# Performance work log

Measured on AMD Instinct MI355X. Metric: run time of the kernel, lower is better.

## Reference

```python
import jax, jax.numpy as jnp
import numpy as np

B, N, F, F1 = 1024, 75, 512, 256
NEG = -1.0e9
ALPHA = 0.2  # LeakyReLU slope


def setup_inputs() -> dict:
    key = jax.random.key(0)
    k1, k2, k3, k4 = jax.random.split(key, 4)
    X = jax.random.normal(k1, (B, N, F), dtype=jnp.float32)
    A = jax.random.randint(k2, (N, N), 0, 2, dtype=jnp.int32)  # binary adjacency
    W = jax.random.normal(k3, (F, F1), dtype=jnp.float32) * (1.0 / np.sqrt(F))
    a = jax.random.normal(k4, (2, F1, 1), dtype=jnp.float32) * (1.0 / np.sqrt(F1))
    return {"X": X, "A": A, "W": W, "a": a}


def reference(X, A, W, a):
    # Linear projection: [B, N, F1]
    h = jnp.einsum('bnf,fo->bno', X, W)
    # Additive attention logits
    att_self = jnp.einsum('bno,od->bnd', h, a[0])        # [B, N, 1]
    att_neigh = jnp.einsum('bno,od->bnd', h, a[1])       # [B, N, 1]
    e = att_self + jnp.swapaxes(att_neigh, 1, 2)         # [B, N, N]
    e = jax.nn.leaky_relu(e, ALPHA)
    # Adjacency mask: disallowed edges get large negative bias
    adj = A.astype(h.dtype)                               # [N, N]
    e = e + NEG * (1.0 - adj)[None, :, :]
    # Normalize over neighbors, aggregate
    alpha = jax.nn.softmax(e, axis=-1)                    # [B, N, N]
    out = jnp.einsum('bij,bjo->bio', alpha, h)            # [B, N, F1]
    return jnp.concatenate([out, h], axis=-1)             # [B, N, 2*F1]
```

## Files before the change

### kernel.cpp

```cpp
#include <hip/hip_runtime.h>
#include <hip/hip_bf16.h>
#include <math.h>

typedef __bf16 bf16_t;
typedef __bf16 bf16x4_t __attribute__((ext_vector_type(4)));
typedef __bf16 bf16x8 __attribute__((ext_vector_type(8)));
typedef float f32x4 __attribute__((ext_vector_type(4)));
typedef unsigned long long u64;

#define NB 1024
#define NN 75
#define KF 512
#define F1 256
#define HSTR 100
#define ASTR 100

__global__ __launch_bounds__(256) void wt_kernel(const float* __restrict__ W,
                                                 bf16_t* __restrict__ Wt) {
    __shared__ float tile[64][65];
    const int kb = blockIdx.x * 64;
    const int nb = blockIdx.y * 64;
    const int tc = threadIdx.x & 63;
    const int tr = threadIdx.x >> 6;
#pragma unroll
    for (int r = tr; r < 64; r += 4)
        tile[r][tc] = W[(size_t)(kb + r) * F1 + nb + tc];
    __syncthreads();
#pragma unroll
    for (int r = tr; r < 64; r += 4)
        Wt[(size_t)(nb + r) * KF + kb + tc] = (bf16_t)tile[tc][r];
}

__global__ __launch_bounds__(256) void gemm_kernel(const float* __restrict__ X,
                                                   const bf16_t* __restrict__ Wt,
                                                   float* __restrict__ out) {
    __shared__ __align__(16) bf16_t Asm[64 * 32];
    __shared__ __align__(16) bf16_t Bsm[256 * 32];
    const int t = threadIdx.x;
    const int w = t >> 6;
    const int l = t & 63;
    const int m0 = blockIdx.x * 64;

    f32x4 acc[16];
#pragma unroll
    for (int i = 0; i < 16; ++i) acc[i] = (f32x4){0.f, 0.f, 0.f, 0.f};

    const int ar = t >> 2;
    const int ak = (t & 3) * 8;
    const float* xptr = X + (size_t)(m0 + ar) * KF + ak;

    const int koff = (l >> 4) * 8;
    const bf16_t* afrag_p = &Asm[(w * 16 + (l & 15)) * 32 + koff];
    const bf16_t* bfrag_p = &Bsm[(l & 15) * 32 + koff];

    for (int ks = 0; ks < 16; ++ks) {
        const int k0 = ks * 32;
        const float4 x0 = *(const float4*)(xptr + k0);
        const float4 x1 = *(const float4*)(xptr + k0 + 4);
        bf16x8 av;
        av[0] = (bf16_t)x0.x; av[1] = (bf16_t)x0.y;
        av[2] = (bf16_t)x0.z; av[3] = (bf16_t)x0.w;
        av[4] = (bf16_t)x1.x; av[5] = (bf16_t)x1.y;
        av[6] = (bf16_t)x1.z; av[7] = (bf16_t)x1.w;
        *(bf16x8*)&Asm[ar * 32 + ak] = av;
#pragma unroll
        for (int p = 0; p < 4; ++p) {
            const int row = p * 64 + ar;
            *(uint4*)&Bsm[row * 32 + ak] =
                *(const uint4*)(Wt + (size_t)row * KF + k0 + ak);
        }
        __syncthreads();
        const bf16x8 af = *(const bf16x8*)afrag_p;
#pragma unroll
        for (int nt = 0; nt < 16; ++nt) {
            const bf16x8 bfv = *(const bf16x8*)(bfrag_p + nt * 16 * 32);
            acc[nt] = __builtin_amdgcn_mfma_f32_16x16x32_bf16(af, bfv, acc[nt], 0, 0, 0);
        }
        __syncthreads();
    }

    const int mrow = m0 + w * 16 + (l >> 4) * 4;
    const int ncol = l & 15;
#pragma unroll
    for (int nt = 0; nt < 16; ++nt) {
#pragma unroll
        for (int j = 0; j < 4; ++j) {
            out[(size_t)(mrow + j) * 512 + 256 + nt * 16 + ncol] = acc[nt][j];
        }
    }
}

__global__ __launch_bounds__(256) void pv_kernel(const int* __restrict__ Adj,
                                                 const float* __restrict__ avec,
                                                 float* __restrict__ out) {
    __shared__ __align__(16) bf16_t hT[256 * HSTR];
    __shared__ __align__(16) bf16_t alp[80 * ASTR];
    __shared__ float a0s[F1], a1s[F1];
    __shared__ float attp0[4][80], attp1[4][80];
    __shared__ float att0s[80], att1s[80], rsums[80];
    __shared__ u64 adjb[160];

    const int b = blockIdx.x;
    const int t = threadIdx.x;
    const int w = t >> 6;
    const int l = t & 63;
    const int lc = l & 15;
    const int lr = l >> 4;
    float* outb = out + (size_t)b * NN * 512;

    a0s[t] = avec[t];
    a1s[t] = avec[F1 + t];
    for (int i = w; i < NN; i += 4) {
        const int v0 = Adj[i * NN + l];
        const int v1 = (l < NN - 64) ? Adj[i * NN + 64 + l] : 0;
        const u64 b0 = __ballot(v0 != 0);
        const u64 b1 = __ballot(v1 != 0);
        if (l == 0) { adjb[i * 2] = b0; adjb[i * 2 + 1] = b1; }
    }
    {
        int* z = (int*)&hT[t * HSTR + 80];
#pragma unroll
        for (int k = 0; k < 8; ++k) z[k] = 0;
    }
    __syncthreads();

    const int c0 = w * 64 + lc * 4;
    const float4 a04 = *(const float4*)&a0s[c0];
    const float4 a14 = *(const float4*)&a1s[c0];
#pragma unroll
    for (int jp = 0; jp < 5; ++jp) {
        const int j0 = jp * 16 + lr * 4;
        float hr[4][4];
#pragma unroll
        for (int r = 0; r < 4; ++r) {
            if (j0 + r < NN) {
                const float4 v = *(const float4*)(outb + (size_t)(j0 + r) * 512 + 256 + c0);
                hr[r][0] = v.x; hr[r][1] = v.y; hr[r][2] = v.z; hr[r][3] = v.w;
            } else {
                hr[r][0] = hr[r][1] = hr[r][2] = hr[r][3] = 0.f;
            }
        }
        float p0[4], p1[4];
#pragma unroll
        for (int r = 0; r < 4; ++r) {
            p0[r] = hr[r][0] * a04.x + hr[r][1] * a04.y + hr[r][2] * a04.z + hr[r][3] * a04.w;
            p1[r] = hr[r][0] * a14.x + hr[r][1] * a14.y + hr[r][2] * a14.z + hr[r][3] * a14.w;
        }
#pragma unroll
        for (int off = 1; off < 16; off <<= 1) {
#pragma unroll
            for (int r = 0; r < 4; ++r) {
                p0[r] += __shfl_xor(p0[r], off);
                p1[r] += __shfl_xor(p1[r], off);
            }
        }
        if (lc == 0) {
#pragma unroll
            for (int r = 0; r < 4; ++r) {
                attp0[w][j0 + r] = p0[r];
                attp1[w][j0 + r] = p1[r];
            }
        }
#pragma unroll
        for (int cc = 0; cc < 4; ++cc) {
            bf16x4_t v;
            v[0] = (bf16_t)hr[0][cc]; v[1] = (bf16_t)hr[1][cc];
            v[2] = (bf16_t)hr[2][cc]; v[3] = (bf16_t)hr[3][cc];
            *(bf16x4_t*)&hT[(c0 + cc) * HSTR + j0] = v;
        }
    }
    __syncthreads();

    if (t < 80)
        att0s[t] = attp0[0][t] + attp0[1][t] + attp0[2][t] + attp0[3][t];
    else if (t < 160)
        att1s[t - 80] = attp1[0][t - 80] + attp1[1][t - 80] + attp1[2][t - 80] + attp1[3][t - 80];
    else if (t < 240) {
        const int r = t - 160;
        if (r < NN) {
            for (int c = NN; c < 96; ++c) alp[r * ASTR + c] = (bf16_t)0.f;
        } else {
            for (int c = 0; c < 96; ++c) alp[r * ASTR + c] = (bf16_t)0.f;
        }
    }
    __syncthreads();

    {
        const int gid = t >> 2;
        const int k4 = t & 3;
#pragma unroll
        for (int r = 0; r < 2; ++r) {
            const int i = r * 64 + gid;
            if (i < NN) {
                const float a0i = att0s[i];
                const u64 w0 = adjb[i * 2];
                const u64 w1 = adjb[i * 2 + 1];
                float e[19];
                float m = -3.0e38f;
#pragma unroll
                for (int jj = 0; jj < 19; ++jj) {
                    const int j = jj * 4 + k4;
                    float ev = -3.0e38f;
                    if (j < NN) {
                        float x = a0i + att1s[j];
                        x = x > 0.f ? x : 0.2f * x;
                        const u64 wj = (j < 64) ? w0 : w1;
                        const int bit = (int)((wj >> (j & 63)) & 1);
                        ev = bit ? x : x - 1.0e9f;
                    }
                    e[jj] = ev;
                    m = fmaxf(m, ev);
                }
                m = fmaxf(m, __shfl_xor(m, 1));
                m = fmaxf(m, __shfl_xor(m, 2));
                float s = 0.f;
#pragma unroll
                for (int jj = 0; jj < 19; ++jj) {
                    const int j = jj * 4 + k4;
                    if (j < NN) {
                        const float ex = __expf(e[jj] - m);
                        s += ex;
                        alp[i * ASTR + j] = (bf16_t)ex;
                    }
                }
                s += __shfl_xor(s, 1);
                s += __shfl_xor(s, 2);
                if (k4 == 0) rsums[i] = 1.f / s;
            }
        }
    }
    __syncthreads();

    f32x4 acc2[5][4];
#pragma unroll
    for (int i = 0; i < 5; ++i)
#pragma unroll
        for (int j = 0; j < 4; ++j) acc2[i][j] = (f32x4){0.f, 0.f, 0.f, 0.f};

#pragma unroll
    for (int ks = 0; ks < 3; ++ks) {
        bf16x8 bv[4];
#pragma unroll
        for (int ntl = 0; ntl < 4; ++ntl) {
            const bf16_t* q = &hT[(w * 64 + ntl * 16 + lc) * HSTR + ks * 32 + lr * 8];
            ((uint2*)&bv[ntl])[0] = *(const uint2*)q;
            ((uint2*)&bv[ntl])[1] = *(const uint2*)(q + 4);
        }
#pragma unroll
        for (int mt = 0; mt < 5; ++mt) {
            const bf16_t* ap = &alp[(mt * 16 + lc) * ASTR + ks * 32 + lr * 8];
            bf16x8 av;
            ((uint2*)&av)[0] = *(const uint2*)ap;
            ((uint2*)&av)[1] = *(const uint2*)(ap + 4);
#pragma unroll
            for (int ntl = 0; ntl < 4; ++ntl)
                acc2[mt][ntl] = __builtin_amdgcn_mfma_f32_16x16x32_bf16(av, bv[ntl], acc2[mt][ntl], 0, 0, 0);
        }
    }

#pragma unroll
    for (int mt = 0; mt < 5; ++mt) {
#pragma unroll
        for (int j = 0; j < 4; ++j) {
            const int row = mt * 16 + lr * 4 + j;
            if (row < NN) {
                const float rsv = rsums[row];
#pragma unroll
                for (int ntl = 0; ntl < 4; ++ntl) {
                    const int ch = w * 64 + ntl * 16 + lc;
                    outb[(size_t)row * 512 + ch] = acc2[mt][ntl][j] * rsv;
                }
            }
        }
    }
}

extern "C" void kernel_launch(void* const* d_in, const int* in_sizes, int n_in,
                              void* d_out, int out_size, void* d_ws, size_t ws_size,
                              hipStream_t stream) {
    const float* X = (const float*)d_in[0];
    const int*   A = (const int*)d_in[1];
    const float* W = (const float*)d_in[2];
    const float* a = (const float*)d_in[3];
    float* out = (float*)d_out;
    bf16_t* Wt = (bf16_t*)d_ws;

    wt_kernel<<<dim3(KF / 64, F1 / 64), 256, 0, stream>>>(W, Wt);
    gemm_kernel<<<(NB * NN) / 64, 256, 0, stream>>>(X, Wt, out);
    pv_kernel<<<NB, 256, 0, stream>>>(A, a, out);
}
```

Before: 136.7 us.

## Double-buffer GEMM shared tiles with register prefetch and fragment-ordered layout

Rewrites the projection GEMM to double-buffer the X and W tiles in shared memory. The next k-slice is prefetched into registers while MFMAs run on the current one, which removes one barrier per iteration. The shared layout is stored in MFMA fragment order so each lane reads contiguous 16-byte chunks without bank conflicts. Each wave now computes a 64x64 tile (4x4 MFMA blocks) instead of 16x256, which reuses A fragments across waves. The cost is more shared memory and more registers, which may reduce occupancy.

```diff
diff --git a/kernel.cpp b/kernel.cpp
--- a/kernel.cpp
+++ b/kernel.cpp
@@ -34,58 +34,98 @@
 __global__ __launch_bounds__(256) void gemm_kernel(const float* __restrict__ X,
                                                    const bf16_t* __restrict__ Wt,
                                                    float* __restrict__ out) {
-    __shared__ __align__(16) bf16_t Asm[64 * 32];
-    __shared__ __align__(16) bf16_t Bsm[256 * 32];
+    __shared__ __align__(16) char smem[40960];
+    bf16_t* Xb = (bf16_t*)smem;
+    bf16_t* Wb = (bf16_t*)(smem + 8192);
+
     const int t = threadIdx.x;
     const int w = t >> 6;
     const int l = t & 63;
+    const int lc = l & 15;
+    const int lr = l >> 4;
     const int m0 = blockIdx.x * 64;
 
-    f32x4 acc[16];
-#pragma unroll
-    for (int i = 0; i < 16; ++i) acc[i] = (f32x4){0.f, 0.f, 0.f, 0.f};
-
-    const int ar = t >> 2;
-    const int ak = (t & 3) * 8;
-    const float* xptr = X + (size_t)(m0 + ar) * KF + ak;
-
-    const int koff = (l >> 4) * 8;
-    const bf16_t* afrag_p = &Asm[(w * 16 + (l & 15)) * 32 + koff];
-    const bf16_t* bfrag_p = &Bsm[(l & 15) * 32 + koff];
+    const int xrow  = ((t >> 6) << 4) + (t & 15);
+    const int kpart = ((t >> 4) & 3) * 8;
+    const float* xsrc = X + (size_t)(m0 + xrow) * KF + kpart;
+    const bf16_t* wsrc0 = Wt + (size_t)(((t >> 6) + 0) * 16 + (t & 15)) * KF + kpart;
+    const bf16_t* wsrc1 = Wt + (size_t)(((t >> 6) + 4) * 16 + (t & 15)) * KF + kpart;
+    const bf16_t* wsrc2 = Wt + (size_t)(((t >> 6) + 8) * 16 + (t & 15)) * KF + kpart;
+    const bf16_t* wsrc3 = Wt + (size_t)(((t >> 6) + 12) * 16 + (t & 15)) * KF + kpart;
+
+    f32x4 acc[4][4];
+#pragma unroll
+    for (int i = 0; i < 4; ++i)
+#pragma unroll
+        for (int j = 0; j < 4; ++j) acc[i][j] = (f32x4){0.f, 0.f, 0.f, 0.f};
+
+    {
+        const float4 xa = *(const float4*)xsrc;
+        const float4 xb = *(const float4*)(xsrc + 4);
+        bf16x8 v;
+        v[0]=(bf16_t)xa.x; v[1]=(bf16_t)xa.y; v[2]=(bf16_t)xa.z; v[3]=(bf16_t)xa.w;
+        v[4]=(bf16_t)xb.x; v[5]=(bf16_t)xb.y; v[6]=(bf16_t)xb.z; v[7]=(bf16_t)xb.w;
+        *(bf16x8*)&Xb[t * 8] = v;
+        *(uint4*)&Wb[t * 8 + 0 * 2048] = *(const uint4*)wsrc0;
+        *(uint4*)&Wb[t * 8 + 1 * 2048] = *(const uint4*)wsrc1;
+        *(uint4*)&Wb[t * 8 + 2 * 2048] = *(const uint4*)wsrc2;
+        *(uint4*)&Wb[t * 8 + 3 * 2048] = *(const uint4*)wsrc3;
+    }
+    __syncthreads();
 
     for (int ks = 0; ks < 16; ++ks) {
-        const int k0 = ks * 32;
-        const float4 x0 = *(const float4*)(xptr + k0);
-        const float4 x1 = *(const float4*)(xptr + k0 + 4);
-        bf16x8 av;
-        av[0] = (bf16_t)x0.x; av[1] = (bf16_t)x0.y;
-        av[2] = (bf16_t)x0.z; av[3] = (bf16_t)x0.w;
-        av[4] = (bf16_t)x1.x; av[5] = (bf16_t)x1.y;
-        av[6] = (bf16_t)x1.z; av[7] = (bf16_t)x1.w;
-        *(bf16x8*)&Asm[ar * 32 + ak] = av;
-#pragma unroll
-        for (int p = 0; p < 4; ++p) {
-            const int row = p * 64 + ar;
-            *(uint4*)&Bsm[row * 32 + ak] =
-                *(const uint4*)(Wt + (size_t)row * KF + k0 + ak);
+        const int cur = ks & 1;
+        float4 xa, xb;
+        uint4 wv0, wv1, wv2, wv3;
+        if (ks < 15) {
+            const int k1 = (ks + 1) * 32;
+            xa = *(const float4*)(xsrc + k1);
+            xb = *(const float4*)(xsrc + k1 + 4);
+            wv0 = *(const uint4*)(wsrc0 + k1);
+            wv1 = *(const uint4*)(wsrc1 + k1);
+            wv2 = *(const uint4*)(wsrc2 + k1);
+            wv3 = *(const uint4*)(wsrc3 + k1);
+        }
+        const bf16_t* Xc = Xb + cur * 2048;
+        const bf16_t* Wc = Wb + cur * 8192;
+        bf16x8 af[4], bv[4];
+#pragma unroll
+        for (int mt = 0; mt < 4; ++mt)
+            af[mt] = *(const bf16x8*)&Xc[(mt * 64 + l) * 8];
+#pragma unroll
+        for (int ntl = 0; ntl < 4; ++ntl)
+            bv[ntl] = *(const bf16x8*)&Wc[((w * 4 + ntl) * 64 + l) * 8];
+#pragma unroll
+        for (int mt = 0; mt < 4; ++mt)
+#pragma unroll
+            for (int ntl = 0; ntl < 4; ++ntl)
+                acc[mt][ntl] = __builtin_amdgcn_mfma_f32_16x16x32_bf16(af[mt], bv[ntl], acc[mt][ntl], 0, 0, 0);
+        if (ks < 15) {
+            const int nxt = cur ^ 1;
+            bf16_t* Xn = Xb + nxt * 2048;
+            bf16_t* Wn = Wb + nxt * 8192;
+            bf16x8 v;
+            v[0]=(bf16_t)xa.x; v[1]=(bf16_t)xa.y; v[2]=(bf16_t)xa.z; v[3]=(bf16_t)xa.w;
+            v[4]=(bf16_t)xb.x; v[5]=(bf16_t)xb.y; v[6]=(bf16_t)xb.z; v[7]=(bf16_t)xb.w;
+            *(bf16x8*)&Xn[t * 8] = v;
+            *(uint4*)&Wn[t * 8 + 0 * 2048] = wv0;
+            *(uint4*)&Wn[t * 8 + 1 * 2048] = wv1;
+            *(uint4*)&Wn[t * 8 + 2 * 2048] = wv2;
+            *(uint4*)&Wn[t * 8 + 3 * 2048] = wv3;
         }
         __syncthreads();
-        const bf16x8 af = *(const bf16x8*)afrag_p;
-#pragma unroll
-        for (int nt = 0; nt < 16; ++nt) {
-            const bf16x8 bfv = *(const bf16x8*)(bfrag_p + nt * 16 * 32);
-            acc[nt] = __builtin_amdgcn_mfma_f32_16x16x32_bf16(af, bfv, acc[nt], 0, 0, 0);
-        }
-        __syncthreads();
-    }
-
-    const int mrow = m0 + w * 16 + (l >> 4) * 4;
-    const int ncol = l & 15;
-#pragma unroll
-    for (int nt = 0; nt < 16; ++nt) {
-#pragma unroll
-        for (int j = 0; j < 4; ++j) {
-            out[(size_t)(mrow + j) * 512 + 256 + nt * 16 + ncol] = acc[nt][j];
+    }
+
+#pragma unroll
+    for (int mt = 0; mt < 4; ++mt) {
+#pragma unroll
+        for (int ntl = 0; ntl < 4; ++ntl) {
+            const int col = w * 64 + ntl * 16 + lc;
+#pragma unroll
+            for (int j = 0; j < 4; ++j) {
+                const int row = m0 + mt * 16 + lr * 4 + j;
+                out[(size_t)row * 512 + 256 + col] = acc[mt][ntl][j];
+            }
         }
     }
 }
```

New measurement: 144.1 us. +5.5%, slower.

## Load GEMM MFMA fragments directly from global memory, dropping LDS staging

Applied to the files above, without the earlier changes.

The projection GEMM no longer stages X and W tiles through shared memory with two barriers per K step. Each lane now loads its MFMA A fragment (X converted to bf16) and its B fragments (Wt) straight from global memory, and the next X fragment is prefetched into registers. The intent is to remove barrier and LDS traffic. In exchange the four waves each read the full W slice independently, relying on L1/L2 hits, and register pressure goes up.

```diff
diff --git a/kernel.cpp b/kernel.cpp
--- a/kernel.cpp
+++ b/kernel.cpp
@@ -34,58 +34,53 @@
 __global__ __launch_bounds__(256) void gemm_kernel(const float* __restrict__ X,
                                                    const bf16_t* __restrict__ Wt,
                                                    float* __restrict__ out) {
-    __shared__ __align__(16) bf16_t Asm[64 * 32];
-    __shared__ __align__(16) bf16_t Bsm[256 * 32];
     const int t = threadIdx.x;
     const int w = t >> 6;
     const int l = t & 63;
+    const int lc = l & 15;
+    const int lr = l >> 4;
     const int m0 = blockIdx.x * 64;
 
+    const float* xsrc = X + (size_t)(m0 + w * 16 + lc) * KF + lr * 8;
+    const bf16_t* wbase = Wt + (size_t)lc * KF + lr * 8;
+
     f32x4 acc[16];
 #pragma unroll
     for (int i = 0; i < 16; ++i) acc[i] = (f32x4){0.f, 0.f, 0.f, 0.f};
 
-    const int ar = t >> 2;
-    const int ak = (t & 3) * 8;
-    const float* xptr = X + (size_t)(m0 + ar) * KF + ak;
-
-    const int koff = (l >> 4) * 8;
-    const bf16_t* afrag_p = &Asm[(w * 16 + (l & 15)) * 32 + koff];
-    const bf16_t* bfrag_p = &Bsm[(l & 15) * 32 + koff];
-
+    float4 xa = *(const float4*)xsrc;
+    float4 xb = *(const float4*)(xsrc + 4);
+
+#pragma unroll
     for (int ks = 0; ks < 16; ++ks) {
-        const int k0 = ks * 32;
-        const float4 x0 = *(const float4*)(xptr + k0);
-        const float4 x1 = *(const float4*)(xptr + k0 + 4);
-        bf16x8 av;
-        av[0] = (bf16_t)x0.x; av[1] = (bf16_t)x0.y;
-        av[2] = (bf16_t)x0.z; av[3] = (bf16_t)x0.w;
-        av[4] = (bf16_t)x1.x; av[5] = (bf16_t)x1.y;
-        av[6] = (bf16_t)x1.z; av[7] = (bf16_t)x1.w;
-        *(bf16x8*)&Asm[ar * 32 + ak] = av;
-#pragma unroll
-        for (int p = 0; p < 4; ++p) {
-            const int row = p * 64 + ar;
-            *(uint4*)&Bsm[row * 32 + ak] =
-                *(const uint4*)(Wt + (size_t)row * KF + k0 + ak);
-        }
-        __syncthreads();
-        const bf16x8 af = *(const bf16x8*)afrag_p;
-#pragma unroll
-        for (int nt = 0; nt < 16; ++nt) {
-            const bf16x8 bfv = *(const bf16x8*)(bfrag_p + nt * 16 * 32);
-            acc[nt] = __builtin_amdgcn_mfma_f32_16x16x32_bf16(af, bfv, acc[nt], 0, 0, 0);
-        }
-        __syncthreads();
-    }
-
-    const int mrow = m0 + w * 16 + (l >> 4) * 4;
-    const int ncol = l & 15;
+        bf16x8 af;
+        af[0] = (bf16_t)xa.x; af[1] = (bf16_t)xa.y;
+        af[2] = (bf16_t)xa.z; af[3] = (bf16_t)xa.w;
+        af[4] = (bf16_t)xb.x; af[5] = (bf16_t)xb.y;
+        af[6] = (bf16_t)xb.z; af[7] = (bf16_t)xb.w;
+        if (ks < 15) {
+            xa = *(const float4*)(xsrc + (ks + 1) * 32);
+            xb = *(const float4*)(xsrc + (ks + 1) * 32 + 4);
+        }
+#pragma unroll
+        for (int h = 0; h < 2; ++h) {
+            bf16x8 wf[8];
+#pragma unroll
+            for (int nt = 0; nt < 8; ++nt)
+                wf[nt] = *(const bf16x8*)(wbase + (size_t)(h * 8 + nt) * 16 * KF + ks * 32);
+#pragma unroll
+            for (int nt = 0; nt < 8; ++nt)
+                acc[h * 8 + nt] = __builtin_amdgcn_mfma_f32_16x16x32_bf16(
+                    af, wf[nt], acc[h * 8 + nt], 0, 0, 0);
+        }
+    }
+
 #pragma unroll
     for (int nt = 0; nt < 16; ++nt) {
 #pragma unroll
         for (int j = 0; j < 4; ++j) {
-            out[(size_t)(mrow + j) * 512 + 256 + nt * 16 + ncol] = acc[nt][j];
+            const int row = m0 + w * 16 + lr * 4 + j;
+            out[(size_t)row * 512 + 256 + nt * 16 + lc] = acc[nt][j];
         }
     }
 }
```

Result: slower. 246.6 us (+80.5%).
